# Optimization experiments

Hardware: AMD Instinct MI355X
Metric: run time of the kernel (lower is better)

Reference implementation:

```python
import jax, jax.numpy as jnp
import numpy as np

N = 50000        # num nodes
E = 1_600_000    # num edges
NNZ = 16         # sparse features per node
V = 100000       # feature vocabulary (num_total_features)
D = 128          # embedding_dim
H = 128          # hidden_dim
O = 64           # out_embedding_dim


def setup_inputs() -> dict:
    key = jax.random.key(0)
    ks = jax.random.split(key, 12)
    s = 0.05
    return {
        "feature_indices": jax.random.randint(ks[0], (N * NNZ,), 0, V, dtype=jnp.int32),
        "feature_offsets": jnp.arange(N, dtype=jnp.int32) * NNZ,
        "feature_weights": jax.random.uniform(ks[1], (N * NNZ,), dtype=jnp.float32),
        "edge_index": jax.random.randint(ks[2], (2, E), 0, N, dtype=jnp.int32),
        "noise": jax.random.normal(ks[3], (N, O), dtype=jnp.float32),
        "emb_table": jax.random.normal(ks[4], (V, D), dtype=jnp.float32) * s,
        "W1": jax.random.normal(ks[5], (D, H), dtype=jnp.float32) * s,
        "b1": jnp.zeros((H,), dtype=jnp.float32),
        "Wmu": jax.random.normal(ks[6], (H, O), dtype=jnp.float32) * s,
        "bmu": jnp.zeros((O,), dtype=jnp.float32),
        "Wls": jax.random.normal(ks[7], (H, O), dtype=jnp.float32) * s,
        "bls": jnp.zeros((O,), dtype=jnp.float32),
    }


def _gcn(x, W, b, src, dst, norm_e, deg_inv):
    # GCNConv with self-loops and symmetric normalization:
    # out_i = sum_{j->i} norm_ji * (W x_j) + deg_i^{-1} * (W x_i) + b
    xw = x @ W
    agg = jax.ops.segment_sum(norm_e[:, None] * xw[src], dst, num_segments=N)
    return agg + xw * deg_inv[:, None] + b


def reference(feature_indices, feature_offsets, feature_weights, edge_index, noise,
              emb_table, W1, b1, Wmu, bmu, Wls, bls):
    # --- EmbeddingBag(mode='sum') with per_sample_weights ---
    total = feature_indices.shape[0]
    bag_ids = jnp.searchsorted(feature_offsets, jnp.arange(total), side="right") - 1
    x = jax.ops.segment_sum(feature_weights[:, None] * emb_table[feature_indices],
                            bag_ids, num_segments=N)  # [N, D]
    # --- F.normalize(p=2, dim=-1) ---
    x = x / jnp.maximum(jnp.linalg.norm(x, axis=-1, keepdims=True), 1e-12)

    # --- shared GCN normalization (self-loops added) ---
    src, dst = edge_index[0], edge_index[1]
    deg = 1.0 + jax.ops.segment_sum(jnp.ones((E,), x.dtype), dst, num_segments=N)
    deg_isqrt = deg ** -0.5
    norm_e = deg_isqrt[src] * deg_isqrt[dst]  # per-edge norm
    deg_inv = 1.0 / deg                        # self-loop norm

    # --- encoder ---
    h = jax.nn.relu(_gcn(x, W1, b1, src, dst, norm_e, deg_inv))
    mu = _gcn(h, Wmu, bmu, src, dst, norm_e, deg_inv)
    logstd = _gcn(h, Wls, bls, src, dst, norm_e, deg_inv)
    z = mu + noise * jnp.exp(logstd)

    # --- dot-product decoder over edge_index ---
    logits = jnp.sum(z[src] * z[dst], axis=-1)  # [E]
    return logits
```

## Files before the change

kernel.cpp:

```cpp
#include <hip/hip_runtime.h>
#include <hip/hip_bf16.h>

constexpr int N_ = 50000;
constexpr int E_ = 1600000;
constexpr int D_ = 128;
constexpr int O_ = 64;
constexpr int NNZ_ = 16;
constexpr int V_ = 100000;
constexpr int NBIN_ = (N_ + 255) / 256;

static __device__ __forceinline__ unsigned short f2bf(float f) {
    __hip_bfloat16 h = __float2bfloat16(f);
    return __builtin_bit_cast(unsigned short, h);
}
static __device__ __forceinline__ float blo(unsigned int u) { return __uint_as_float(u << 16); }
static __device__ __forceinline__ float bhi(unsigned int u) { return __uint_as_float(u & 0xffff0000u); }
static __device__ __forceinline__ float4 fma4(float s, float4 a, float4 b) {
    return make_float4(fmaf(s, a.x, b.x), fmaf(s, a.y, b.y),
                       fmaf(s, a.z, b.z), fmaf(s, a.w, b.w));
}

__global__ __launch_bounds__(256) void k_cvt(const float* __restrict__ emb,
                                             unsigned int* __restrict__ emb_bf) {
    int t = blockIdx.x * blockDim.x + threadIdx.x;
    if (t >= V_ * D_ / 8) return;
    float4 a = ((const float4*)emb)[t * 2];
    float4 b = ((const float4*)emb)[t * 2 + 1];
    uint4 o;
    o.x = (unsigned int)f2bf(a.x) | ((unsigned int)f2bf(a.y) << 16);
    o.y = (unsigned int)f2bf(a.z) | ((unsigned int)f2bf(a.w) << 16);
    o.z = (unsigned int)f2bf(b.x) | ((unsigned int)f2bf(b.y) << 16);
    o.w = (unsigned int)f2bf(b.z) | ((unsigned int)f2bf(b.w) << 16);
    ((uint4*)emb_bf)[t] = o;
}

__global__ __launch_bounds__(256) void k_embed(const int* __restrict__ fi,
                                               const float* __restrict__ fw,
                                               const unsigned int* __restrict__ emb_bf,
                                               unsigned int* __restrict__ x) {
    int n = blockIdx.x * 4 + (threadIdx.x >> 6);
    if (n >= N_) return;
    int lane = threadIdx.x & 63;
    float a0 = 0.f, a1 = 0.f;
    int base = n * NNZ_;
#pragma unroll
    for (int j = 0; j < NNZ_; ++j) {
        int idx  = fi[base + j];
        float w  = fw[base + j];
        unsigned int r = emb_bf[(size_t)idx * 64 + lane];
        a0 = fmaf(w, blo(r), a0);
        a1 = fmaf(w, bhi(r), a1);
    }
    float ss = a0 * a0 + a1 * a1;
#pragma unroll
    for (int o = 32; o; o >>= 1) ss += __shfl_xor(ss, o);
    float sc = 1.0f / fmaxf(sqrtf(ss), 1e-12f);
    x[(size_t)n * 64 + lane] =
        (unsigned int)f2bf(a0 * sc) | ((unsigned int)f2bf(a1 * sc) << 16);
}

__global__ __launch_bounds__(256) void k_degcnt(const int* __restrict__ dst,
                                                int* __restrict__ cnt) {
    int e = blockIdx.x * blockDim.x + threadIdx.x;
    if (e < E_) atomicAdd(&cnt[dst[e]], 1);
}

__global__ __launch_bounds__(256) void k_degnorm(const int* __restrict__ cnt,
                                                 float* __restrict__ disq,
                                                 float* __restrict__ dinv) {
    int n = blockIdx.x * blockDim.x + threadIdx.x;
    if (n < N_) {
        float deg = 1.0f + (float)cnt[n];
        disq[n] = rsqrtf(deg);
        dinv[n] = 1.0f / deg;
    }
}

__global__ __launch_bounds__(256) void k_bsum(const int* __restrict__ cnt,
                                              int* __restrict__ bsum) {
    int t = threadIdx.x, n = (blockIdx.x << 8) + t;
    int v = (n < N_) ? cnt[n] : 0;
#pragma unroll
    for (int o = 32; o; o >>= 1) v += __shfl_xor(v, o);
    __shared__ int ws[4];
    if ((t & 63) == 0) ws[t >> 6] = v;
    __syncthreads();
    if (t == 0) bsum[blockIdx.x] = ws[0] + ws[1] + ws[2] + ws[3];
}

__global__ __launch_bounds__(256) void k_scan196(const int* __restrict__ bsum,
                                                 int* __restrict__ coarse_start,
                                                 int* __restrict__ coarse_cursor,
                                                 int* __restrict__ row_start) {
    __shared__ int s[256];
    int t = threadIdx.x;
    int v = (t < NBIN_) ? bsum[t] : 0;
    s[t] = v;
    __syncthreads();
    for (int o = 1; o < 256; o <<= 1) {
        int u = (t >= o) ? s[t - o] : 0;
        __syncthreads();
        s[t] += u;
        __syncthreads();
    }
    int excl = s[t] - v;
    if (t <= NBIN_) { coarse_start[t] = excl; coarse_cursor[t] = excl; }
    if (t == 0) row_start[N_] = E_;
}

__global__ __launch_bounds__(256) void k_rowstart(const int* __restrict__ cnt,
                                                  const int* __restrict__ coarse_start,
                                                  int* __restrict__ row_start) {
    __shared__ int s[256];
    int t = threadIdx.x, n = (blockIdx.x << 8) + t;
    int v = (n < N_) ? cnt[n] : 0;
    s[t] = v;
    __syncthreads();
    for (int o = 1; o < 256; o <<= 1) {
        int u = (t >= o) ? s[t - o] : 0;
        __syncthreads();
        s[t] += u;
        __syncthreads();
    }
    if (n < N_) row_start[n] = coarse_start[blockIdx.x] + (s[t] - v);
}

constexpr int EPB_ = 4096;
__global__ __launch_bounds__(256) void k_bin(const int* __restrict__ src,
                                             const int* __restrict__ dst,
                                             int* __restrict__ coarse_cursor,
                                             uint2* __restrict__ binned) {
    __shared__ int hist[256], base[256];
    int t = threadIdx.x;
    int e0 = blockIdx.x * EPB_;
    hist[t] = 0;
    __syncthreads();
#pragma unroll
    for (int i = 0; i < EPB_ / 256; ++i) {
        int e = e0 + i * 256 + t;
        if (e < E_) atomicAdd(&hist[dst[e] >> 8], 1);
    }
    __syncthreads();
    if (t < NBIN_ && hist[t]) base[t] = atomicAdd(&coarse_cursor[t], hist[t]);
    __syncthreads();
#pragma unroll
    for (int i = 0; i < EPB_ / 256; ++i) {
        int e = e0 + i * 256 + t;
        if (e < E_) {
            int d = dst[e];
            int pos = atomicAdd(&base[d >> 8], 1);
            binned[pos] = make_uint2((unsigned int)src[e], (unsigned int)d);
        }
    }
}

__global__ __launch_bounds__(256) void k_fill2(const uint2* __restrict__ binned,
                                               const int* __restrict__ coarse_start,
                                               const int* __restrict__ row_start,
                                               int* __restrict__ sorted_src) {
    __shared__ int cur[256];
    int t = threadIdx.x;
    int n0 = blockIdx.x << 8;
    if (n0 + t < N_) cur[t] = row_start[n0 + t];
    __syncthreads();
    int beg = coarse_start[blockIdx.x], end = coarse_start[blockIdx.x + 1];
    for (int j = beg + t; j < end; j += 256) {
        uint2 e = binned[j];
        int pos = atomicAdd(&cur[e.y - (unsigned int)n0], 1);
        sorted_src[pos] = (int)e.x;
    }
}

__global__ __launch_bounds__(256) void k_gather(const int* __restrict__ row_start,
                                                const int* __restrict__ sorted_src,
                                                const float* __restrict__ disq,
                                                const float* __restrict__ dinv,
                                                const unsigned int* __restrict__ v,
                                                float* __restrict__ agg) {
    int n = blockIdx.x * 4 + (threadIdx.x >> 6);
    if (n >= N_) return;
    int lane = threadIdx.x & 63;
    int beg = row_start[n], end = row_start[n + 1];
    float ax = 0.f, ay = 0.f;
    int j = beg;
    for (; j + 7 < end; j += 8) {
        int s0 = sorted_src[j],     s1 = sorted_src[j + 1];
        int s2 = sorted_src[j + 2], s3 = sorted_src[j + 3];
        int s4 = sorted_src[j + 4], s5 = sorted_src[j + 5];
        int s6 = sorted_src[j + 6], s7 = sorted_src[j + 7];
        float w0 = disq[s0], w1 = disq[s1], w2 = disq[s2], w3 = disq[s3];
        float w4 = disq[s4], w5 = disq[s5], w6 = disq[s6], w7 = disq[s7];
        unsigned int b0 = v[(size_t)s0 * 64 + lane];
        unsigned int b1 = v[(size_t)s1 * 64 + lane];
        unsigned int b2 = v[(size_t)s2 * 64 + lane];
        unsigned int b3 = v[(size_t)s3 * 64 + lane];
        unsigned int b4 = v[(size_t)s4 * 64 + lane];
        unsigned int b5 = v[(size_t)s5 * 64 + lane];
        unsigned int b6 = v[(size_t)s6 * 64 + lane];
        unsigned int b7 = v[(size_t)s7 * 64 + lane];
        ax = fmaf(w0, blo(b0), ax); ay = fmaf(w0, bhi(b0), ay);
        ax = fmaf(w1, blo(b1), ax); ay = fmaf(w1, bhi(b1), ay);
        ax = fmaf(w2, blo(b2), ax); ay = fmaf(w2, bhi(b2), ay);
        ax = fmaf(w3, blo(b3), ax); ay = fmaf(w3, bhi(b3), ay);
        ax = fmaf(w4, blo(b4), ax); ay = fmaf(w4, bhi(b4), ay);
        ax = fmaf(w5, blo(b5), ax); ay = fmaf(w5, bhi(b5), ay);
        ax = fmaf(w6, blo(b6), ax); ay = fmaf(w6, bhi(b6), ay);
        ax = fmaf(w7, blo(b7), ax); ay = fmaf(w7, bhi(b7), ay);
    }
    for (; j < end; ++j) {
        int s = sorted_src[j];
        float w = disq[s];
        unsigned int b = v[(size_t)s * 64 + lane];
        ax = fmaf(w, blo(b), ax); ay = fmaf(w, bhi(b), ay);
    }
    float dq = disq[n], di = dinv[n];
    unsigned int bs = v[(size_t)n * 64 + lane];
    ax = fmaf(di, blo(bs), ax * dq);
    ay = fmaf(di, bhi(bs), ay * dq);
    ((float2*)agg)[(size_t)n * 64 + lane] = make_float2(ax, ay);
}

__global__ __launch_bounds__(256, 2) void k_gemm_relu(const float* __restrict__ u,
                                                      const float* __restrict__ W,
                                                      const float* __restrict__ b,
                                                      unsigned short* __restrict__ hout) {
    __shared__ float lw[D_ * D_];
    __shared__ float lu[32 * D_];
    int tid = threadIdx.x;
    for (int t = tid; t < D_ * D_ / 4; t += 256)
        ((float4*)lw)[t] = ((const float4*)W)[t];

    int l  = tid & 31;
    int rl = ((tid >> 6) << 3) + (((tid >> 5) & 1) << 2);
    float4 bb = ((const float4*)b)[l];

    for (int tile = blockIdx.x; tile * 32 < N_; tile += gridDim.x) {
        int row0 = tile * 32;
        __syncthreads();
#pragma unroll
        for (int i = 0; i < 4; ++i) {
            int flat = i * 256 + tid;
            int r = flat >> 5, c4 = flat & 31;
            int gr = row0 + r;
            ((float4*)lu)[flat] = (gr < N_) ? ((const float4*)u)[(size_t)gr * 32 + c4]
                                            : make_float4(0.f, 0.f, 0.f, 0.f);
        }
        __syncthreads();
        float4 a0 = {0,0,0,0}, a1 = {0,0,0,0}, a2 = {0,0,0,0}, a3 = {0,0,0,0};
#pragma unroll 4
        for (int k4 = 0; k4 < 32; ++k4) {
            int k = k4 * 4;
            float4 w0 = ((const float4*)(lw + (k + 0) * D_))[l];
            float4 w1 = ((const float4*)(lw + (k + 1) * D_))[l];
            float4 w2 = ((const float4*)(lw + (k + 2) * D_))[l];
            float4 w3 = ((const float4*)(lw + (k + 3) * D_))[l];
            float4 u0 = ((const float4*)(lu + (rl + 0) * D_))[k4];
            float4 u1 = ((const float4*)(lu + (rl + 1) * D_))[k4];
            float4 u2 = ((const float4*)(lu + (rl + 2) * D_))[k4];
            float4 u3 = ((const float4*)(lu + (rl + 3) * D_))[k4];
            a0 = fma4(u0.x, w0, fma4(u0.y, w1, fma4(u0.z, w2, fma4(u0.w, w3, a0))));
            a1 = fma4(u1.x, w0, fma4(u1.y, w1, fma4(u1.z, w2, fma4(u1.w, w3, a1))));
            a2 = fma4(u2.x, w0, fma4(u2.y, w1, fma4(u2.z, w2, fma4(u2.w, w3, a2))));
            a3 = fma4(u3.x, w0, fma4(u3.y, w1, fma4(u3.z, w2, fma4(u3.w, w3, a3))));
        }
        float4 accs[4] = {a0, a1, a2, a3};
#pragma unroll
        for (int r = 0; r < 4; ++r) {
            int row = row0 + rl + r;
            if (row < N_) {
                float4 a = accs[r];
                ushort4 o;
                o.x = f2bf(fmaxf(a.x + bb.x, 0.f));
                o.y = f2bf(fmaxf(a.y + bb.y, 0.f));
                o.z = f2bf(fmaxf(a.z + bb.z, 0.f));
                o.w = f2bf(fmaxf(a.w + bb.w, 0.f));
                ((ushort4*)hout)[(size_t)row * 32 + l] = o;
            }
        }
    }
}

__global__ __launch_bounds__(256, 2) void k_gemm_z(const float* __restrict__ g,
                                                   const float* __restrict__ Wmu,
                                                   const float* __restrict__ bmu,
                                                   const float* __restrict__ Wls,
                                                   const float* __restrict__ bls,
                                                   const float* __restrict__ noise,
                                                   unsigned int* __restrict__ z) {
    __shared__ float lw[D_ * D_];
    __shared__ float lu[32 * D_];
    int tid = threadIdx.x;
    for (int t = tid; t < D_ * 32; t += 256) {
        int k = t >> 5, j2 = t & 31;
        float2 m2 = ((const float2*)Wmu)[k * 32 + j2];
        float2 l2 = ((const float2*)Wls)[k * 32 + j2];
        ((float4*)lw)[t] = make_float4(m2.x, l2.x, m2.y, l2.y);
    }

    int l  = tid & 31;
    int rl = ((tid >> 6) << 3) + (((tid >> 5) & 1) << 2);
    float2 bm = ((const float2*)bmu)[l];
    float2 bl = ((const float2*)bls)[l];
    float4 bb = make_float4(bm.x, bl.x, bm.y, bl.y);

    for (int tile = blockIdx.x; tile * 32 < N_; tile += gridDim.x) {
        int row0 = tile * 32;
        __syncthreads();
#pragma unroll
        for (int i = 0; i < 4; ++i) {
            int flat = i * 256 + tid;
            int r = flat >> 5, c4 = flat & 31;
            int gr = row0 + r;
            ((float4*)lu)[flat] = (gr < N_) ? ((const float4*)g)[(size_t)gr * 32 + c4]
                                            : make_float4(0.f, 0.f, 0.f, 0.f);
        }
        __syncthreads();
        float4 a0 = {0,0,0,0}, a1 = {0,0,0,0}, a2 = {0,0,0,0}, a3 = {0,0,0,0};
#pragma unroll 4
        for (int k4 = 0; k4 < 32; ++k4) {
            int k = k4 * 4;
            float4 w0 = ((const float4*)(lw + (k + 0) * D_))[l];
            float4 w1 = ((const float4*)(lw + (k + 1) * D_))[l];
            float4 w2 = ((const float4*)(lw + (k + 2) * D_))[l];
            float4 w3 = ((const float4*)(lw + (k + 3) * D_))[l];
            float4 u0 = ((const float4*)(lu + (rl + 0) * D_))[k4];
            float4 u1 = ((const float4*)(lu + (rl + 1) * D_))[k4];
            float4 u2 = ((const float4*)(lu + (rl + 2) * D_))[k4];
            float4 u3 = ((const float4*)(lu + (rl + 3) * D_))[k4];
            a0 = fma4(u0.x, w0, fma4(u0.y, w1, fma4(u0.z, w2, fma4(u0.w, w3, a0))));
            a1 = fma4(u1.x, w0, fma4(u1.y, w1, fma4(u1.z, w2, fma4(u1.w, w3, a1))));
            a2 = fma4(u2.x, w0, fma4(u2.y, w1, fma4(u2.z, w2, fma4(u2.w, w3, a2))));
            a3 = fma4(u3.x, w0, fma4(u3.y, w1, fma4(u3.z, w2, fma4(u3.w, w3, a3))));
        }
        float4 accs[4] = {a0, a1, a2, a3};
#pragma unroll
        for (int r = 0; r < 4; ++r) {
            int row = row0 + rl + r;
            if (row < N_) {
                float4 a = accs[r];
                float2 n2 = ((const float2*)noise)[(size_t)row * 32 + l];
                float z0 = (a.x + bb.x) + n2.x * expf(a.y + bb.y);
                float z1 = (a.z + bb.z) + n2.y * expf(a.w + bb.w);
                z[(size_t)row * 32 + l] =
                    (unsigned int)f2bf(z0) | ((unsigned int)f2bf(z1) << 16);
            }
        }
    }
}

__global__ __launch_bounds__(256) void k_decode(const int* __restrict__ src,
                                                const int* __restrict__ dst,
                                                const unsigned int* __restrict__ z,
                                                float* __restrict__ out) {
    int e = blockIdx.x * 16 + (threadIdx.x >> 4);
    if (e >= E_) return;
    int l = threadIdx.x & 15;
    int s = src[e], d = dst[e];
    uint2 za = ((const uint2*)z)[(size_t)s * 16 + l];
    uint2 zb = ((const uint2*)z)[(size_t)d * 16 + l];
    float p = blo(za.x) * blo(zb.x) + bhi(za.x) * bhi(zb.x)
            + blo(za.y) * blo(zb.y) + bhi(za.y) * bhi(zb.y);
#pragma unroll
    for (int o = 8; o; o >>= 1) p += __shfl_xor(p, o);
    if (l == 0) out[e] = p;
}

extern "C" void kernel_launch(void* const* d_in, const int* in_sizes, int n_in,
                              void* d_out, int out_size, void* d_ws, size_t ws_size,
                              hipStream_t stream) {
    const int*   fi    = (const int*)d_in[0];
    const float* fw    = (const float*)d_in[2];
    const int*   ei    = (const int*)d_in[3];
    const float* noise = (const float*)d_in[4];
    const float* emb   = (const float*)d_in[5];
    const float* W1    = (const float*)d_in[6];
    const float* b1    = (const float*)d_in[7];
    const float* Wmu   = (const float*)d_in[8];
    const float* bmu   = (const float*)d_in[9];
    const float* Wls   = (const float*)d_in[10];
    const float* bls   = (const float*)d_in[11];
    float* out = (float*)d_out;

    const int* src = ei;
    const int* dst = ei + E_;

    float*        ws        = (float*)d_ws;
    float*        agg       = ws;
    unsigned int* emb_bf    = (unsigned int*)agg;
    uint2*        binned    = (uint2*)agg;
    unsigned int* x         = (unsigned int*)(agg + (size_t)N_ * D_);
    unsigned int* h         = x + (size_t)N_ * 64;
    unsigned int* z         = h + (size_t)N_ * 64;
    float*        disq      = (float*)(z + (size_t)N_ * 32);
    float*        dinv      = disq + N_;
    int*          cnt       = (int*)(dinv + N_);
    int*          row_start = cnt + N_;
    int*          sorted_src= row_start + (N_ + 1);
    int*          bsum      = sorted_src + E_;
    int*          coarse_start  = bsum + 256;
    int*          coarse_cursor = coarse_start + 256;

    hipMemsetAsync(cnt, 0, N_ * sizeof(int), stream);

    k_cvt    <<<(V_ * D_ / 8 + 255) / 256, 256, 0, stream>>>(emb, emb_bf);
    k_embed  <<<N_ / 4,            256, 0, stream>>>(fi, fw, emb_bf, x);
    k_degcnt <<<(E_ + 255) / 256,  256, 0, stream>>>(dst, cnt);
    k_degnorm<<<(N_ + 255) / 256,  256, 0, stream>>>(cnt, disq, dinv);
    k_bsum   <<<NBIN_,             256, 0, stream>>>(cnt, bsum);
    k_scan196<<<1,                 256, 0, stream>>>(bsum, coarse_start, coarse_cursor,
                                                     row_start);
    k_rowstart<<<NBIN_,            256, 0, stream>>>(cnt, coarse_start, row_start);
    k_bin    <<<(E_ + EPB_ - 1) / EPB_, 256, 0, stream>>>(src, dst, coarse_cursor, binned);
    k_fill2  <<<NBIN_,             256, 0, stream>>>(binned, coarse_start, row_start,
                                                     sorted_src);

    k_gather   <<<N_ / 4, 256, 0, stream>>>(row_start, sorted_src, disq, dinv, x, agg);
    k_gemm_relu<<<512,    256, 0, stream>>>(agg, W1, b1, (unsigned short*)h);

    k_gather <<<N_ / 4,   256, 0, stream>>>(row_start, sorted_src, disq, dinv, h, agg);
    k_gemm_z <<<512,      256, 0, stream>>>(agg, Wmu, bmu, Wls, bls, noise, z);

    k_decode <<<E_ / 16,  256, 0, stream>>>(src, dst, z, out);
}
```

Before: 540.9 us.

## Split neighbor gather and decoder into column-slice passes for cache locality

```diff
diff --git a/kernel.cpp b/kernel.cpp
--- a/kernel.cpp
+++ b/kernel.cpp
@@ -171,53 +171,49 @@
     }
 }
 
-__global__ __launch_bounds__(256) void k_gather(const int* __restrict__ row_start,
-                                                const int* __restrict__ sorted_src,
-                                                const float* __restrict__ disq,
-                                                const float* __restrict__ dinv,
-                                                const unsigned int* __restrict__ v,
-                                                float* __restrict__ agg) {
+template<int Q>
+__global__ __launch_bounds__(256) void k_gather_q(const int* __restrict__ row_start,
+                                                  const int* __restrict__ sorted_src,
+                                                  const float* __restrict__ disq,
+                                                  const float* __restrict__ dinv,
+                                                  const unsigned int* __restrict__ v,
+                                                  float2* __restrict__ agg) {
     int n = blockIdx.x * 4 + (threadIdx.x >> 6);
     if (n >= N_) return;
     int lane = threadIdx.x & 63;
+    int jj = lane >> 4, c = lane & 15;
+    int col = Q * 16 + c;
     int beg = row_start[n], end = row_start[n + 1];
     float ax = 0.f, ay = 0.f;
-    int j = beg;
-    for (; j + 7 < end; j += 8) {
-        int s0 = sorted_src[j],     s1 = sorted_src[j + 1];
-        int s2 = sorted_src[j + 2], s3 = sorted_src[j + 3];
-        int s4 = sorted_src[j + 4], s5 = sorted_src[j + 5];
-        int s6 = sorted_src[j + 6], s7 = sorted_src[j + 7];
+    int j = beg + jj;
+    for (; j + 12 < end; j += 16) {
+        int s0 = sorted_src[j],      s1 = sorted_src[j + 4];
+        int s2 = sorted_src[j + 8],  s3 = sorted_src[j + 12];
         float w0 = disq[s0], w1 = disq[s1], w2 = disq[s2], w3 = disq[s3];
-        float w4 = disq[s4], w5 = disq[s5], w6 = disq[s6], w7 = disq[s7];
-        unsigned int b0 = v[(size_t)s0 * 64 + lane];
-        unsigned int b1 = v[(size_t)s1 * 64 + lane];
-        unsigned int b2 = v[(size_t)s2 * 64 + lane];
-        unsigned int b3 = v[(size_t)s3 * 64 + lane];
-        unsigned int b4 = v[(size_t)s4 * 64 + lane];
-        unsigned int b5 = v[(size_t)s5 * 64 + lane];
-        unsigned int b6 = v[(size_t)s6 * 64 + lane];
-        unsigned int b7 = v[(size_t)s7 * 64 + lane];
+        unsigned int b0 = v[(size_t)s0 * 64 + col];
+        unsigned int b1 = v[(size_t)s1 * 64 + col];
+        unsigned int b2 = v[(size_t)s2 * 64 + col];
+        unsigned int b3 = v[(size_t)s3 * 64 + col];
         ax = fmaf(w0, blo(b0), ax); ay = fmaf(w0, bhi(b0), ay);
         ax = fmaf(w1, blo(b1), ax); ay = fmaf(w1, bhi(b1), ay);
         ax = fmaf(w2, blo(b2), ax); ay = fmaf(w2, bhi(b2), ay);
         ax = fmaf(w3, blo(b3), ax); ay = fmaf(w3, bhi(b3), ay);
-        ax = fmaf(w4, blo(b4), ax); ay = fmaf(w4, bhi(b4), ay);
-        ax = fmaf(w5, blo(b5), ax); ay = fmaf(w5, bhi(b5), ay);
-        ax = fmaf(w6, blo(b6), ax); ay = fmaf(w6, bhi(b6), ay);
-        ax = fmaf(w7, blo(b7), ax); ay = fmaf(w7, bhi(b7), ay);
-    }
-    for (; j < end; ++j) {
+    }
+    for (; j < end; j += 4) {
         int s = sorted_src[j];
         float w = disq[s];
-        unsigned int b = v[(size_t)s * 64 + lane];
+        unsigned int b = v[(size_t)s * 64 + col];
         ax = fmaf(w, blo(b), ax); ay = fmaf(w, bhi(b), ay);
     }
-    float dq = disq[n], di = dinv[n];
-    unsigned int bs = v[(size_t)n * 64 + lane];
-    ax = fmaf(di, blo(bs), ax * dq);
-    ay = fmaf(di, bhi(bs), ay * dq);
-    ((float2*)agg)[(size_t)n * 64 + lane] = make_float2(ax, ay);
+    ax += __shfl_xor(ax, 16); ax += __shfl_xor(ax, 32);
+    ay += __shfl_xor(ay, 16); ay += __shfl_xor(ay, 32);
+    if (jj == 0) {
+        float dq = disq[n], di = dinv[n];
+        unsigned int bs = v[(size_t)n * 64 + col];
+        float rx = fmaf(di, blo(bs), ax * dq);
+        float ry = fmaf(di, bhi(bs), ay * dq);
+        agg[(size_t)n * 64 + col] = make_float2(rx, ry);
+    }
 }
 
 __global__ __launch_bounds__(256, 2) void k_gemm_relu(const float* __restrict__ u,
@@ -348,21 +344,22 @@
     }
 }
 
-__global__ __launch_bounds__(256) void k_decode(const int* __restrict__ src,
-                                                const int* __restrict__ dst,
-                                                const unsigned int* __restrict__ z,
-                                                float* __restrict__ out) {
-    int e = blockIdx.x * 16 + (threadIdx.x >> 4);
+template<int HALF>
+__global__ __launch_bounds__(256) void k_decode_h(const int* __restrict__ src,
+                                                  const int* __restrict__ dst,
+                                                  const unsigned int* __restrict__ z,
+                                                  float* __restrict__ out) {
+    int e = blockIdx.x * 32 + (threadIdx.x >> 3);
     if (e >= E_) return;
-    int l = threadIdx.x & 15;
+    int l = threadIdx.x & 7;
     int s = src[e], d = dst[e];
-    uint2 za = ((const uint2*)z)[(size_t)s * 16 + l];
-    uint2 zb = ((const uint2*)z)[(size_t)d * 16 + l];
+    uint2 za = ((const uint2*)z)[(size_t)s * 16 + HALF * 8 + l];
+    uint2 zb = ((const uint2*)z)[(size_t)d * 16 + HALF * 8 + l];
     float p = blo(za.x) * blo(zb.x) + bhi(za.x) * bhi(zb.x)
             + blo(za.y) * blo(zb.y) + bhi(za.y) * bhi(zb.y);
 #pragma unroll
-    for (int o = 8; o; o >>= 1) p += __shfl_xor(p, o);
-    if (l == 0) out[e] = p;
+    for (int o = 4; o; o >>= 1) p += __shfl_xor(p, o);
+    if (l == 0) out[e] = HALF ? out[e] + p : p;
 }
 
 extern "C" void kernel_launch(void* const* d_in, const int* in_sizes, int n_in,
@@ -414,11 +411,18 @@
     k_fill2  <<<NBIN_,             256, 0, stream>>>(binned, coarse_start, row_start,
                                                      sorted_src);
 
-    k_gather   <<<N_ / 4, 256, 0, stream>>>(row_start, sorted_src, disq, dinv, x, agg);
-    k_gemm_relu<<<512,    256, 0, stream>>>(agg, W1, b1, (unsigned short*)h);
-
-    k_gather <<<N_ / 4,   256, 0, stream>>>(row_start, sorted_src, disq, dinv, h, agg);
-    k_gemm_z <<<512,      256, 0, stream>>>(agg, Wmu, bmu, Wls, bls, noise, z);
-
-    k_decode <<<E_ / 16,  256, 0, stream>>>(src, dst, z, out);
-}
+    k_gather_q<0><<<N_ / 4, 256, 0, stream>>>(row_start, sorted_src, disq, dinv, x, (float2*)agg);
+    k_gather_q<1><<<N_ / 4, 256, 0, stream>>>(row_start, sorted_src, disq, dinv, x, (float2*)agg);
+    k_gather_q<2><<<N_ / 4, 256, 0, stream>>>(row_start, sorted_src, disq, dinv, x, (float2*)agg);
+    k_gather_q<3><<<N_ / 4, 256, 0, stream>>>(row_start, sorted_src, disq, dinv, x, (float2*)agg);
+    k_gemm_relu<<<512,      256, 0, stream>>>(agg, W1, b1, (unsigned short*)h);
+
+    k_gather_q<0><<<N_ / 4, 256, 0, stream>>>(row_start, sorted_src, disq, dinv, h, (float2*)agg);
+    k_gather_q<1><<<N_ / 4, 256, 0, stream>>>(row_start, sorted_src, disq, dinv, h, (float2*)agg);
+    k_gather_q<2><<<N_ / 4, 256, 0, stream>>>(row_start, sorted_src, disq, dinv, h, (float2*)agg);
+    k_gather_q<3><<<N_ / 4, 256, 0, stream>>>(row_start, sorted_src, disq, dinv, h, (float2*)agg);
+    k_gemm_z <<<512,        256, 0, stream>>>(agg, Wmu, bmu, Wls, bls, noise, z);
+
+    k_decode_h<0><<<E_ / 32, 256, 0, stream>>>(src, dst, z, out);
+    k_decode_h<1><<<E_ / 32, 256, 0, stream>>>(src, dst, z, out);
+}
```

Result: slower. 678.9 us (+25.5%).

## Derive degrees and row starts from coarse binning, pack binned edges to 32 bits

Applied to the files above, without the earlier changes.

```diff
diff --git a/kernel.cpp b/kernel.cpp
--- a/kernel.cpp
+++ b/kernel.cpp
@@ -59,42 +59,30 @@
         (unsigned int)f2bf(a0 * sc) | ((unsigned int)f2bf(a1 * sc) << 16);
 }
 
-__global__ __launch_bounds__(256) void k_degcnt(const int* __restrict__ dst,
-                                                int* __restrict__ cnt) {
-    int e = blockIdx.x * blockDim.x + threadIdx.x;
-    if (e < E_) atomicAdd(&cnt[dst[e]], 1);
-}
-
-__global__ __launch_bounds__(256) void k_degnorm(const int* __restrict__ cnt,
-                                                 float* __restrict__ disq,
-                                                 float* __restrict__ dinv) {
-    int n = blockIdx.x * blockDim.x + threadIdx.x;
-    if (n < N_) {
-        float deg = 1.0f + (float)cnt[n];
-        disq[n] = rsqrtf(deg);
-        dinv[n] = 1.0f / deg;
-    }
-}
-
-__global__ __launch_bounds__(256) void k_bsum(const int* __restrict__ cnt,
-                                              int* __restrict__ bsum) {
-    int t = threadIdx.x, n = (blockIdx.x << 8) + t;
-    int v = (n < N_) ? cnt[n] : 0;
-#pragma unroll
-    for (int o = 32; o; o >>= 1) v += __shfl_xor(v, o);
-    __shared__ int ws[4];
-    if ((t & 63) == 0) ws[t >> 6] = v;
-    __syncthreads();
-    if (t == 0) bsum[blockIdx.x] = ws[0] + ws[1] + ws[2] + ws[3];
-}
-
-__global__ __launch_bounds__(256) void k_scan196(const int* __restrict__ bsum,
+constexpr int EPB_ = 4096;
+__global__ __launch_bounds__(256) void k_bhist(const int* __restrict__ dst,
+                                               int* __restrict__ bin_total) {
+    __shared__ int hist[256];
+    int t = threadIdx.x;
+    hist[t] = 0;
+    __syncthreads();
+    int e0 = blockIdx.x * EPB_;
+#pragma unroll
+    for (int i = 0; i < EPB_ / 256; ++i) {
+        int e = e0 + i * 256 + t;
+        if (e < E_) atomicAdd(&hist[dst[e] >> 8], 1);
+    }
+    __syncthreads();
+    if (t < NBIN_ && hist[t]) atomicAdd(&bin_total[t], hist[t]);
+}
+
+__global__ __launch_bounds__(256) void k_scan196(const int* __restrict__ bin_total,
                                                  int* __restrict__ coarse_start,
                                                  int* __restrict__ coarse_cursor,
                                                  int* __restrict__ row_start) {
     __shared__ int s[256];
     int t = threadIdx.x;
-    int v = (t < NBIN_) ? bsum[t] : 0;
+    int v = (t < NBIN_) ? bin_total[t] : 0;
     s[t] = v;
     __syncthreads();
     for (int o = 1; o < 256; o <<= 1) {
@@ -108,28 +96,10 @@
     if (t == 0) row_start[N_] = E_;
 }
 
-__global__ __launch_bounds__(256) void k_rowstart(const int* __restrict__ cnt,
-                                                  const int* __restrict__ coarse_start,
-                                                  int* __restrict__ row_start) {
-    __shared__ int s[256];
-    int t = threadIdx.x, n = (blockIdx.x << 8) + t;
-    int v = (n < N_) ? cnt[n] : 0;
-    s[t] = v;
-    __syncthreads();
-    for (int o = 1; o < 256; o <<= 1) {
-        int u = (t >= o) ? s[t - o] : 0;
-        __syncthreads();
-        s[t] += u;
-        __syncthreads();
-    }
-    if (n < N_) row_start[n] = coarse_start[blockIdx.x] + (s[t] - v);
-}
-
-constexpr int EPB_ = 4096;
 __global__ __launch_bounds__(256) void k_bin(const int* __restrict__ src,
                                              const int* __restrict__ dst,
                                              int* __restrict__ coarse_cursor,
-                                             uint2* __restrict__ binned) {
+                                             unsigned int* __restrict__ binned) {
     __shared__ int hist[256], base[256];
     int t = threadIdx.x;
     int e0 = blockIdx.x * EPB_;
@@ -149,12 +119,43 @@
         if (e < E_) {
             int d = dst[e];
             int pos = atomicAdd(&base[d >> 8], 1);
-            binned[pos] = make_uint2((unsigned int)src[e], (unsigned int)d);
-        }
-    }
-}
-
-__global__ __launch_bounds__(256) void k_fill2(const uint2* __restrict__ binned,
+            binned[pos] = (unsigned int)src[e] | ((unsigned int)(d & 255) << 16);
+        }
+    }
+}
+
+__global__ __launch_bounds__(256) void k_node(const unsigned int* __restrict__ binned,
+                                              const int* __restrict__ coarse_start,
+                                              float* __restrict__ disq,
+                                              float* __restrict__ dinv,
+                                              int* __restrict__ row_start) {
+    __shared__ int hist[256], s[256];
+    int t = threadIdx.x;
+    hist[t] = 0;
+    __syncthreads();
+    int beg = coarse_start[blockIdx.x], end = coarse_start[blockIdx.x + 1];
+    for (int j = beg + t; j < end; j += 256)
+        atomicAdd(&hist[(binned[j] >> 16) & 255], 1);
+    __syncthreads();
+    int v = hist[t];
+    int n = (blockIdx.x << 8) + t;
+    if (n < N_) {
+        float deg = 1.0f + (float)v;
+        disq[n] = rsqrtf(deg);
+        dinv[n] = 1.0f / deg;
+    }
+    s[t] = v;
+    __syncthreads();
+    for (int o = 1; o < 256; o <<= 1) {
+        int u = (t >= o) ? s[t - o] : 0;
+        __syncthreads();
+        s[t] += u;
+        __syncthreads();
+    }
+    if (n < N_) row_start[n] = beg + (s[t] - v);
+}
+
+__global__ __launch_bounds__(256) void k_fill2(const unsigned int* __restrict__ binned,
                                                const int* __restrict__ coarse_start,
                                                const int* __restrict__ row_start,
                                                int* __restrict__ sorted_src) {
@@ -165,9 +166,9 @@
     __syncthreads();
     int beg = coarse_start[blockIdx.x], end = coarse_start[blockIdx.x + 1];
     for (int j = beg + t; j < end; j += 256) {
-        uint2 e = binned[j];
-        int pos = atomicAdd(&cur[e.y - (unsigned int)n0], 1);
-        sorted_src[pos] = (int)e.x;
+        unsigned int b = binned[j];
+        int pos = atomicAdd(&cur[(b >> 16) & 255], 1);
+        sorted_src[pos] = (int)(b & 0xFFFFu);
     }
 }
 
@@ -387,32 +388,30 @@
     float*        ws        = (float*)d_ws;
     float*        agg       = ws;
     unsigned int* emb_bf    = (unsigned int*)agg;
-    uint2*        binned    = (uint2*)agg;
+    unsigned int* binned    = (unsigned int*)agg;
     unsigned int* x         = (unsigned int*)(agg + (size_t)N_ * D_);
     unsigned int* h         = x + (size_t)N_ * 64;
     unsigned int* z         = h + (size_t)N_ * 64;
     float*        disq      = (float*)(z + (size_t)N_ * 32);
     float*        dinv      = disq + N_;
-    int*          cnt       = (int*)(dinv + N_);
-    int*          row_start = cnt + N_;
+    int*          row_start = (int*)(dinv + N_);
     int*          sorted_src= row_start + (N_ + 1);
-    int*          bsum      = sorted_src + E_;
-    int*          coarse_start  = bsum + 256;
+    int*          bin_total = sorted_src + E_;
+    int*          coarse_start  = bin_total + 256;
     int*          coarse_cursor = coarse_start + 256;
 
-    hipMemsetAsync(cnt, 0, N_ * sizeof(int), stream);
+    hipMemsetAsync(bin_total, 0, 256 * sizeof(int), stream);
 
     k_cvt    <<<(V_ * D_ / 8 + 255) / 256, 256, 0, stream>>>(emb, emb_bf);
-    k_embed  <<<N_ / 4,            256, 0, stream>>>(fi, fw, emb_bf, x);
-    k_degcnt <<<(E_ + 255) / 256,  256, 0, stream>>>(dst, cnt);
-    k_degnorm<<<(N_ + 255) / 256,  256, 0, stream>>>(cnt, disq, dinv);
-    k_bsum   <<<NBIN_,             256, 0, stream>>>(cnt, bsum);
-    k_scan196<<<1,                 256, 0, stream>>>(bsum, coarse_start, coarse_cursor,
-                                                     row_start);
-    k_rowstart<<<NBIN_,            256, 0, stream>>>(cnt, coarse_start, row_start);
+    k_embed  <<<N_ / 4,                 256, 0, stream>>>(fi, fw, emb_bf, x);
+    k_bhist  <<<(E_ + EPB_ - 1) / EPB_, 256, 0, stream>>>(dst, bin_total);
+    k_scan196<<<1,                      256, 0, stream>>>(bin_total, coarse_start,
+                                                          coarse_cursor, row_start);
     k_bin    <<<(E_ + EPB_ - 1) / EPB_, 256, 0, stream>>>(src, dst, coarse_cursor, binned);
-    k_fill2  <<<NBIN_,             256, 0, stream>>>(binned, coarse_start, row_start,
-                                                     sorted_src);
+    k_node   <<<NBIN_,                  256, 0, stream>>>(binned, coarse_start,
+                                                          disq, dinv, row_start);
+    k_fill2  <<<NBIN_,                  256, 0, stream>>>(binned, coarse_start,
+                                                          row_start, sorted_src);
 
     k_gather   <<<N_ / 4, 256, 0, stream>>>(row_start, sorted_src, disq, dinv, x, agg);
     k_gemm_relu<<<512,    256, 0, stream>>>(agg, W1, b1, (unsigned short*)h);
```

Measured after the change: 489.8 us. 1.1x faster.
